# Performance work log

Hardware: AMD Instinct MI355X
Metric: run time of the kernel (lower is better)

The kernel has to match this reference:

```python
import jax, jax.numpy as jnp
import numpy as np

H = 16  # n_heads

def setup_inputs() -> dict:
    key = jax.random.key(0)
    ks = jax.random.split(key, 7)
    B, L, D = 4, 2048, 1024
    s = 0.02
    return {
        "z": jax.random.normal(ks[0], (B, L, D), jnp.float32),
        "connection": jax.random.normal(ks[1], (B, L, D), jnp.float32),
        "Wq": jax.random.normal(ks[2], (2 * D, D), jnp.float32) * s,
        "Wk": jax.random.normal(ks[3], (2 * D, D), jnp.float32) * s,
        "Wv": jax.random.normal(ks[4], (D, D), jnp.float32) * s,
        "Wo": jax.random.normal(ks[5], (D, D), jnp.float32) * s,
        "temp": jnp.float32(1.0),
    }

def reference(z, connection, Wq, Wk, Wv, Wo, temp):
    B, L, D = z.shape
    hd = D // H
    zc = jnp.concatenate([z, connection], axis=-1)          # [B,L,2D]
    Q = (zc @ Wq).reshape(B, L, H, hd).transpose(0, 2, 1, 3)  # [B,H,L,hd]
    K = (zc @ Wk).reshape(B, L, H, hd).transpose(0, 2, 1, 3)
    V = (z @ Wv).reshape(B, L, H, hd).transpose(0, 2, 1, 3)
    scale = (hd ** -0.5) * temp
    scores = jnp.einsum('bhqd,bhkd->bhqk', Q, K) * scale     # [B,H,L,L]
    rel = jax.nn.sigmoid(scores)
    rel_sum = jnp.clip(rel.sum(-1, keepdims=True), 1.0, None)
    out = jnp.einsum('bhqk,bhkd->bhqd', rel, V) / rel_sum
    out = out.transpose(0, 2, 1, 3).reshape(B, L, D)
    return out @ Wo
```

## Files before the change

### kernel.cpp

```cpp
#include <hip/hip_runtime.h>

typedef unsigned short u16;
typedef unsigned int u32;
typedef __bf16 bf16x8 __attribute__((ext_vector_type(8)));
typedef float f32x4 __attribute__((ext_vector_type(4)));

#define DEV static __device__ __forceinline__

DEV u16 f2bf(float x) {
    union { float f; u32 u; } v; v.f = x;
    u32 r = (v.u + 0x7FFFu + ((v.u >> 16) & 1u)) >> 16;
    return (u16)r;
}

DEV void store_c(float* p, float v) { *p = v; }
DEV void store_c(u16* p, float v) { *p = f2bf(v); }

DEV int swz(int row, int bytecol) { return row * 128 + (bytecol ^ ((row & 7) << 4)); }

__global__ void pack_zc(const float* __restrict__ z, const float* __restrict__ cn,
                        u16* __restrict__ zc) {
    size_t i = ((size_t)blockIdx.x * blockDim.x + threadIdx.x) * 4;
    size_t t = i >> 11;
    int c = (int)(i & 2047);
    const float* src = (c < 1024) ? (z + t * 1024 + c) : (cn + t * 1024 + (c - 1024));
    float4 v = *reinterpret_cast<const float4*>(src);
    u32 lo = (u32)f2bf(v.x) | ((u32)f2bf(v.y) << 16);
    u32 hi = (u32)f2bf(v.z) | ((u32)f2bf(v.w) << 16);
    *reinterpret_cast<uint2*>(zc + i) = make_uint2(lo, hi);
}

__global__ void transpose_conv_w(const float* __restrict__ W, u16* __restrict__ WT,
                                 int K, int N) {
    __shared__ float tile[32][33];
    int n0 = blockIdx.x * 32, k0 = blockIdx.y * 32;
    int tx = threadIdx.x, ty = threadIdx.y;
    #pragma unroll
    for (int i = ty; i < 32; i += 8)
        tile[i][tx] = W[(size_t)(k0 + i) * N + n0 + tx];
    __syncthreads();
    #pragma unroll
    for (int i = ty; i < 32; i += 8)
        WT[(size_t)(n0 + i) * K + k0 + tx] = f2bf(tile[tx][i]);
}

__global__ void transpose_v(const u16* __restrict__ Vf, u16* __restrict__ Vt) {
    __shared__ u16 tile[32][33];
    int bh = blockIdx.z; int b = bh >> 4, h = bh & 15;
    int l0 = blockIdx.x * 32, d0 = blockIdx.y * 32;
    int tx = threadIdx.x, ty = threadIdx.y;
    #pragma unroll
    for (int i = ty; i < 32; i += 8)
        tile[i][tx] = Vf[(size_t)(b * 2048 + l0 + i) * 1024 + h * 64 + d0 + tx];
    __syncthreads();
    #pragma unroll
    for (int i = ty; i < 32; i += 8)
        Vt[((size_t)bh * 64 + d0 + i) * 2048 + l0 + tx] = tile[tx][i];
}

template <typename OutT>
__global__ __launch_bounds__(256, 2)
void gemm_bt(const u16* __restrict__ A, const u16* __restrict__ BT,
             OutT* __restrict__ C, int M, int N, int K,
             int lda, int ldb, int ldc) {
    __shared__ u16 As[128 * 64];
    __shared__ u16 Bs[128 * 64];
    const int tid = threadIdx.x;
    const int lane = tid & 63;
    const int wid = tid >> 6;
    const int m0 = blockIdx.x * 128;
    const int n0 = blockIdx.y * 128;
    const int wr = (wid >> 1) * 64;
    const int wc = (wid & 1) * 64;

    f32x4 acc[4][4];
    #pragma unroll
    for (int i = 0; i < 4; ++i)
        #pragma unroll
        for (int j = 0; j < 4; ++j)
            acc[i][j] = f32x4{0.f, 0.f, 0.f, 0.f};

    const int srow = tid >> 3;
    const int schunk = tid & 7;

    for (int k0 = 0; k0 < K; k0 += 64) {
        __syncthreads();
        #pragma unroll
        for (int p = 0; p < 4; ++p) {
            int row = p * 32 + srow;
            int4 v = *reinterpret_cast<const int4*>(A + (size_t)(m0 + row) * lda + k0 + schunk * 8);
            *reinterpret_cast<int4*>(reinterpret_cast<char*>(As) + swz(row, schunk * 16)) = v;
        }
        #pragma unroll
        for (int p = 0; p < 4; ++p) {
            int row = p * 32 + srow;
            int4 v = *reinterpret_cast<const int4*>(BT + (size_t)(n0 + row) * ldb + k0 + schunk * 8);
            *reinterpret_cast<int4*>(reinterpret_cast<char*>(Bs) + swz(row, schunk * 16)) = v;
        }
        __syncthreads();
        #pragma unroll
        for (int kk = 0; kk < 64; kk += 32) {
            bf16x8 af[4], bfr[4];
            #pragma unroll
            for (int i = 0; i < 4; ++i) {
                int row = wr + i * 16 + (lane & 15);
                af[i] = *reinterpret_cast<const bf16x8*>(
                    reinterpret_cast<const char*>(As) + swz(row, (kk + (lane >> 4) * 8) * 2));
            }
            #pragma unroll
            for (int j = 0; j < 4; ++j) {
                int row = wc + j * 16 + (lane & 15);
                bfr[j] = *reinterpret_cast<const bf16x8*>(
                    reinterpret_cast<const char*>(Bs) + swz(row, (kk + (lane >> 4) * 8) * 2));
            }
            #pragma unroll
            for (int i = 0; i < 4; ++i)
                #pragma unroll
                for (int j = 0; j < 4; ++j)
                    acc[i][j] = __builtin_amdgcn_mfma_f32_16x16x32_bf16(af[i], bfr[j], acc[i][j], 0, 0, 0);
        }
    }

    #pragma unroll
    for (int i = 0; i < 4; ++i)
        #pragma unroll
        for (int j = 0; j < 4; ++j)
            #pragma unroll
            for (int r = 0; r < 4; ++r) {
                int row = m0 + wr + i * 16 + (lane >> 4) * 4 + r;
                int col = n0 + wc + j * 16 + (lane & 15);
                store_c(&C[(size_t)row * ldc + col], acc[i][j][r]);
            }
}

__global__ __launch_bounds__(256, 2)
void attn_kernel(const u16* __restrict__ Qf, const u16* __restrict__ Kf,
                 const u16* __restrict__ Vt, u16* __restrict__ Oa,
                 const float* __restrict__ temp) {
    constexpr int L = 2048, D = 1024, HD = 64;
    __shared__ u16 Qs[64 * 64];
    __shared__ u16 Ks[64 * 64];
    __shared__ u16 Vs[64 * 64];
    __shared__ u16 Ps[4][16 * 64];

    const int tid = threadIdx.x;
    const int lane = tid & 63;
    const int wid = tid >> 6;
    const int bh = blockIdx.y;
    const int b = bh >> 4, h = bh & 15;
    const int q0 = blockIdx.x * 64;
    const float scale = temp[0] * 0.125f;

    const u16* Qbase = Qf + (size_t)(b * L) * D + h * HD;
    const u16* Kbase = Kf + (size_t)(b * L) * D + h * HD;
    const u16* Vbase = Vt + (size_t)bh * HD * L;

    const int srow = tid >> 3;
    const int schunk = tid & 7;

    #pragma unroll
    for (int p = 0; p < 2; ++p) {
        int row = p * 32 + srow;
        int4 v = *reinterpret_cast<const int4*>(Qbase + (size_t)(q0 + row) * D + schunk * 8);
        *reinterpret_cast<int4*>(reinterpret_cast<char*>(Qs) + swz(row, schunk * 16)) = v;
    }

    f32x4 oacc[4];
    #pragma unroll
    for (int j = 0; j < 4; ++j) oacc[j] = f32x4{0.f, 0.f, 0.f, 0.f};
    float rsum[4] = {0.f, 0.f, 0.f, 0.f};

    for (int k0 = 0; k0 < L; k0 += 64) {
        __syncthreads();
        #pragma unroll
        for (int p = 0; p < 2; ++p) {
            int row = p * 32 + srow;
            int4 v = *reinterpret_cast<const int4*>(Kbase + (size_t)(k0 + row) * D + schunk * 8);
            *reinterpret_cast<int4*>(reinterpret_cast<char*>(Ks) + swz(row, schunk * 16)) = v;
        }
        #pragma unroll
        for (int p = 0; p < 2; ++p) {
            int row = p * 32 + srow;
            int4 v = *reinterpret_cast<const int4*>(Vbase + (size_t)row * L + k0 + schunk * 8);
            *reinterpret_cast<int4*>(reinterpret_cast<char*>(Vs) + swz(row, schunk * 16)) = v;
        }
        __syncthreads();

        f32x4 s[4];
        #pragma unroll
        for (int ct = 0; ct < 4; ++ct) s[ct] = f32x4{0.f, 0.f, 0.f, 0.f};
        #pragma unroll
        for (int kk = 0; kk < 64; kk += 32) {
            int qrow = wid * 16 + (lane & 15);
            bf16x8 aq = *reinterpret_cast<const bf16x8*>(
                reinterpret_cast<const char*>(Qs) + swz(qrow, (kk + (lane >> 4) * 8) * 2));
            #pragma unroll
            for (int ct = 0; ct < 4; ++ct) {
                int krow = ct * 16 + (lane & 15);
                bf16x8 bk = *reinterpret_cast<const bf16x8*>(
                    reinterpret_cast<const char*>(Ks) + swz(krow, (kk + (lane >> 4) * 8) * 2));
                s[ct] = __builtin_amdgcn_mfma_f32_16x16x32_bf16(aq, bk, s[ct], 0, 0, 0);
            }
        }

        #pragma unroll
        for (int ct = 0; ct < 4; ++ct) {
            #pragma unroll
            for (int r = 0; r < 4; ++r) {
                float pv = 1.0f / (1.0f + __expf(-s[ct][r] * scale));
                rsum[r] += pv;
                int prow = (lane >> 4) * 4 + r;
                *reinterpret_cast<u16*>(reinterpret_cast<char*>(Ps[wid]) +
                    swz(prow, (ct * 16 + (lane & 15)) * 2)) = f2bf(pv);
            }
        }

        #pragma unroll
        for (int kk = 0; kk < 64; kk += 32) {
            int prow = (lane & 15);
            bf16x8 ap = *reinterpret_cast<const bf16x8*>(
                reinterpret_cast<const char*>(Ps[wid]) + swz(prow, (kk + (lane >> 4) * 8) * 2));
            #pragma unroll
            for (int ct = 0; ct < 4; ++ct) {
                int vrow = ct * 16 + (lane & 15);
                bf16x8 bv = *reinterpret_cast<const bf16x8*>(
                    reinterpret_cast<const char*>(Vs) + swz(vrow, (kk + (lane >> 4) * 8) * 2));
                oacc[ct] = __builtin_amdgcn_mfma_f32_16x16x32_bf16(ap, bv, oacc[ct], 0, 0, 0);
            }
        }
    }

    #pragma unroll
    for (int r = 0; r < 4; ++r) {
        float v = rsum[r];
        v += __shfl_xor(v, 1);
        v += __shfl_xor(v, 2);
        v += __shfl_xor(v, 4);
        v += __shfl_xor(v, 8);
        rsum[r] = fmaxf(v, 1.0f);
    }

    #pragma unroll
    for (int ct = 0; ct < 4; ++ct)
        #pragma unroll
        for (int r = 0; r < 4; ++r) {
            int row = q0 + wid * 16 + (lane >> 4) * 4 + r;
            int col = h * HD + ct * 16 + (lane & 15);
            Oa[(size_t)(b * L + row) * D + col] = f2bf(oacc[ct][r] / rsum[r]);
        }
}

extern "C" void kernel_launch(void* const* d_in, const int* in_sizes, int n_in,
                              void* d_out, int out_size, void* d_ws, size_t ws_size,
                              hipStream_t stream) {
    const float* z    = (const float*)d_in[0];
    const float* cn   = (const float*)d_in[1];
    const float* Wq   = (const float*)d_in[2];
    const float* Wk   = (const float*)d_in[3];
    const float* Wv   = (const float*)d_in[4];
    const float* Wo   = (const float*)d_in[5];
    const float* temp = (const float*)d_in[6];

    char* ws = (char*)d_ws;
    u16* zc  = (u16*)ws; ws += (size_t)8192 * 2048 * 2;
    u16* WqT = (u16*)ws; ws += (size_t)1024 * 2048 * 2;
    u16* WkT = (u16*)ws; ws += (size_t)1024 * 2048 * 2;
    u16* WvT = (u16*)ws; ws += (size_t)1024 * 1024 * 2;
    u16* WoT = (u16*)ws; ws += (size_t)1024 * 1024 * 2;
    u16* Qf  = (u16*)ws; ws += (size_t)8192 * 1024 * 2;
    u16* Kf  = (u16*)ws; ws += (size_t)8192 * 1024 * 2;
    u16* Vf  = (u16*)ws; ws += (size_t)8192 * 1024 * 2;
    u16* Vt  = zc;
    u16* Oa  = Vf;

    pack_zc<<<16384, 256, 0, stream>>>(z, cn, zc);

    dim3 tb(32, 8);
    transpose_conv_w<<<dim3(32, 64), tb, 0, stream>>>(Wq, WqT, 2048, 1024);
    transpose_conv_w<<<dim3(32, 64), tb, 0, stream>>>(Wk, WkT, 2048, 1024);
    transpose_conv_w<<<dim3(32, 32), tb, 0, stream>>>(Wv, WvT, 1024, 1024);
    transpose_conv_w<<<dim3(32, 32), tb, 0, stream>>>(Wo, WoT, 1024, 1024);

    gemm_bt<u16><<<dim3(64, 8), 256, 0, stream>>>(zc, WqT, Qf, 8192, 1024, 2048, 2048, 2048, 1024);
    gemm_bt<u16><<<dim3(64, 8), 256, 0, stream>>>(zc, WkT, Kf, 8192, 1024, 2048, 2048, 2048, 1024);
    gemm_bt<u16><<<dim3(64, 8), 256, 0, stream>>>(zc, WvT, Vf, 8192, 1024, 1024, 2048, 1024, 1024);

    transpose_v<<<dim3(64, 2, 64), tb, 0, stream>>>(Vf, Vt);

    attn_kernel<<<dim3(32, 64), 256, 0, stream>>>(Qf, Kf, Vt, Oa, temp);

    gemm_bt<float><<<dim3(64, 8), 256, 0, stream>>>(Oa, WoT, (float*)d_out, 8192, 1024, 1024, 1024, 1024, 1024);
}
```

Measured before the change: 476.3 us.

## Use direct global-to-LDS loads, fuse Q/K GEMM, and compute row sums with MFMA

GEMM and attention tile loads now use global_load_lds into a pre-swizzled LDS layout instead of going through registers. The Q and K projections become one GEMM with N=2048, since WqT and WkT sit next to each other in the workspace; attention reads Q and K from that interleaved buffer. The sigmoid now uses exp2 and a hardware reciprocal. Row sums come from an extra MFMA against a ones vector, which removes the shuffle reduction, and manual bf16 rounding is replaced by native conversions. The MFMA row sum is taken over bf16-rounded probabilities, so precision shifts slightly, and correctness relies on the barrier waiting for the async LDS loads.

```diff
diff --git a/kernel.cpp b/kernel.cpp
--- a/kernel.cpp
+++ b/kernel.cpp
@@ -7,14 +7,14 @@
 
 #define DEV static __device__ __forceinline__
 
-DEV u16 f2bf(float x) {
-    union { float f; u32 u; } v; v.f = x;
-    u32 r = (v.u + 0x7FFFu + ((v.u >> 16) & 1u)) >> 16;
-    return (u16)r;
+DEV void gload16(const void* g, void* l) {
+    __builtin_amdgcn_global_load_lds(
+        (const __attribute__((address_space(1))) void*)g,
+        (__attribute__((address_space(3))) void*)l, 16, 0, 0);
 }
 
 DEV void store_c(float* p, float v) { *p = v; }
-DEV void store_c(u16* p, float v) { *p = f2bf(v); }
+DEV void store_c(u16* p, float v) { *(__bf16*)p = (__bf16)v; }
 
 DEV int swz(int row, int bytecol) { return row * 128 + (bytecol ^ ((row & 7) << 4)); }
 
@@ -25,9 +25,10 @@
     int c = (int)(i & 2047);
     const float* src = (c < 1024) ? (z + t * 1024 + c) : (cn + t * 1024 + (c - 1024));
     float4 v = *reinterpret_cast<const float4*>(src);
-    u32 lo = (u32)f2bf(v.x) | ((u32)f2bf(v.y) << 16);
-    u32 hi = (u32)f2bf(v.z) | ((u32)f2bf(v.w) << 16);
-    *reinterpret_cast<uint2*>(zc + i) = make_uint2(lo, hi);
+    union { __bf16 h[4]; uint2 u; } o;
+    o.h[0] = (__bf16)v.x; o.h[1] = (__bf16)v.y;
+    o.h[2] = (__bf16)v.z; o.h[3] = (__bf16)v.w;
+    *reinterpret_cast<uint2*>(zc + i) = o.u;
 }
 
 __global__ void transpose_conv_w(const float* __restrict__ W, u16* __restrict__ WT,
@@ -41,7 +42,7 @@
     __syncthreads();
     #pragma unroll
     for (int i = ty; i < 32; i += 8)
-        WT[(size_t)(n0 + i) * K + k0 + tx] = f2bf(tile[tx][i]);
+        *(__bf16*)&WT[(size_t)(n0 + i) * K + k0 + tx] = (__bf16)tile[tx][i];
 }
 
 __global__ void transpose_v(const u16* __restrict__ Vf, u16* __restrict__ Vt) {
@@ -80,24 +81,25 @@
         for (int j = 0; j < 4; ++j)
             acc[i][j] = f32x4{0.f, 0.f, 0.f, 0.f};
 
-    const int srow = tid >> 3;
-    const int schunk = tid & 7;
+    const int srcoff = ((lane & 7) ^ (lane >> 3)) * 8;
+    const int rb = wid * 32 + (lane >> 3);
+    const u16* aptr[4]; const u16* bptr[4];
+    #pragma unroll
+    for (int p = 0; p < 4; ++p) {
+        aptr[p] = A  + (size_t)(m0 + rb + p * 8) * lda + srcoff;
+        bptr[p] = BT + (size_t)(n0 + rb + p * 8) * ldb + srcoff;
+    }
 
     for (int k0 = 0; k0 < K; k0 += 64) {
         __syncthreads();
         #pragma unroll
-        for (int p = 0; p < 4; ++p) {
-            int row = p * 32 + srow;
-            int4 v = *reinterpret_cast<const int4*>(A + (size_t)(m0 + row) * lda + k0 + schunk * 8);
-            *reinterpret_cast<int4*>(reinterpret_cast<char*>(As) + swz(row, schunk * 16)) = v;
-        }
-        #pragma unroll
-        for (int p = 0; p < 4; ++p) {
-            int row = p * 32 + srow;
-            int4 v = *reinterpret_cast<const int4*>(BT + (size_t)(n0 + row) * ldb + k0 + schunk * 8);
-            *reinterpret_cast<int4*>(reinterpret_cast<char*>(Bs) + swz(row, schunk * 16)) = v;
-        }
-        __syncthreads();
+        for (int p = 0; p < 4; ++p)
+            gload16(aptr[p] + k0, (char*)As + (wid * 4 + p) * 1024);
+        #pragma unroll
+        for (int p = 0; p < 4; ++p)
+            gload16(bptr[p] + k0, (char*)Bs + (wid * 4 + p) * 1024);
+        __syncthreads();
+
         #pragma unroll
         for (int kk = 0; kk < 64; kk += 32) {
             bf16x8 af[4], bfr[4];
@@ -134,10 +136,9 @@
 }
 
 __global__ __launch_bounds__(256, 2)
-void attn_kernel(const u16* __restrict__ Qf, const u16* __restrict__ Kf,
-                 const u16* __restrict__ Vt, u16* __restrict__ Oa,
-                 const float* __restrict__ temp) {
-    constexpr int L = 2048, D = 1024, HD = 64;
+void attn_kernel(const u16* __restrict__ QKf, const u16* __restrict__ Vt,
+                 u16* __restrict__ Oa, const float* __restrict__ temp) {
+    constexpr int L = 2048, D = 1024, QKLD = 2048, HD = 64;
     __shared__ u16 Qs[64 * 64];
     __shared__ u16 Ks[64 * 64];
     __shared__ u16 Vs[64 * 64];
@@ -149,41 +150,44 @@
     const int bh = blockIdx.y;
     const int b = bh >> 4, h = bh & 15;
     const int q0 = blockIdx.x * 64;
-    const float scale = temp[0] * 0.125f;
-
-    const u16* Qbase = Qf + (size_t)(b * L) * D + h * HD;
-    const u16* Kbase = Kf + (size_t)(b * L) * D + h * HD;
+    const float sneg = -temp[0] * 0.125f * 1.44269504f;
+
+    const u16* Qbase = QKf + (size_t)(b * L) * QKLD + h * HD;
+    const u16* Kbase = Qbase + 1024;
     const u16* Vbase = Vt + (size_t)bh * HD * L;
 
-    const int srow = tid >> 3;
-    const int schunk = tid & 7;
-
+    const int srcoff = ((lane & 7) ^ (lane >> 3)) * 8;
+    const int rb = wid * 16 + (lane >> 3);
+
+    #pragma unroll
+    for (int p = 0; p < 2; ++p)
+        gload16(Qbase + (size_t)(q0 + rb + p * 8) * QKLD + srcoff,
+                (char*)Qs + (wid * 2 + p) * 1024);
+
+    const u16* kptr[2]; const u16* vptr[2];
     #pragma unroll
     for (int p = 0; p < 2; ++p) {
-        int row = p * 32 + srow;
-        int4 v = *reinterpret_cast<const int4*>(Qbase + (size_t)(q0 + row) * D + schunk * 8);
-        *reinterpret_cast<int4*>(reinterpret_cast<char*>(Qs) + swz(row, schunk * 16)) = v;
-    }
+        kptr[p] = Kbase + (size_t)(rb + p * 8) * QKLD + srcoff;
+        vptr[p] = Vbase + (size_t)(rb + p * 8) * L + srcoff;
+    }
+
+    bf16x8 onesf;
+    #pragma unroll
+    for (int j = 0; j < 8; ++j) onesf[j] = (__bf16)1.0f;
 
     f32x4 oacc[4];
     #pragma unroll
     for (int j = 0; j < 4; ++j) oacc[j] = f32x4{0.f, 0.f, 0.f, 0.f};
-    float rsum[4] = {0.f, 0.f, 0.f, 0.f};
+    f32x4 racc = f32x4{0.f, 0.f, 0.f, 0.f};
 
     for (int k0 = 0; k0 < L; k0 += 64) {
         __syncthreads();
         #pragma unroll
-        for (int p = 0; p < 2; ++p) {
-            int row = p * 32 + srow;
-            int4 v = *reinterpret_cast<const int4*>(Kbase + (size_t)(k0 + row) * D + schunk * 8);
-            *reinterpret_cast<int4*>(reinterpret_cast<char*>(Ks) + swz(row, schunk * 16)) = v;
-        }
-        #pragma unroll
-        for (int p = 0; p < 2; ++p) {
-            int row = p * 32 + srow;
-            int4 v = *reinterpret_cast<const int4*>(Vbase + (size_t)row * L + k0 + schunk * 8);
-            *reinterpret_cast<int4*>(reinterpret_cast<char*>(Vs) + swz(row, schunk * 16)) = v;
-        }
+        for (int p = 0; p < 2; ++p)
+            gload16(kptr[p] + (size_t)k0 * QKLD, (char*)Ks + (wid * 2 + p) * 1024);
+        #pragma unroll
+        for (int p = 0; p < 2; ++p)
+            gload16(vptr[p] + k0, (char*)Vs + (wid * 2 + p) * 1024);
         __syncthreads();
 
         f32x4 s[4];
@@ -207,11 +211,10 @@
         for (int ct = 0; ct < 4; ++ct) {
             #pragma unroll
             for (int r = 0; r < 4; ++r) {
-                float pv = 1.0f / (1.0f + __expf(-s[ct][r] * scale));
-                rsum[r] += pv;
+                float pv = __builtin_amdgcn_rcpf(1.0f + exp2f(s[ct][r] * sneg));
                 int prow = (lane >> 4) * 4 + r;
-                *reinterpret_cast<u16*>(reinterpret_cast<char*>(Ps[wid]) +
-                    swz(prow, (ct * 16 + (lane & 15)) * 2)) = f2bf(pv);
+                *(__bf16*)(reinterpret_cast<char*>(Ps[wid]) +
+                    swz(prow, (ct * 16 + (lane & 15)) * 2)) = (__bf16)pv;
             }
         }
 
@@ -220,6 +223,7 @@
             int prow = (lane & 15);
             bf16x8 ap = *reinterpret_cast<const bf16x8*>(
                 reinterpret_cast<const char*>(Ps[wid]) + swz(prow, (kk + (lane >> 4) * 8) * 2));
+            racc = __builtin_amdgcn_mfma_f32_16x16x32_bf16(ap, onesf, racc, 0, 0, 0);
             #pragma unroll
             for (int ct = 0; ct < 4; ++ct) {
                 int vrow = ct * 16 + (lane & 15);
@@ -230,15 +234,10 @@
         }
     }
 
-    #pragma unroll
-    for (int r = 0; r < 4; ++r) {
-        float v = rsum[r];
-        v += __shfl_xor(v, 1);
-        v += __shfl_xor(v, 2);
-        v += __shfl_xor(v, 4);
-        v += __shfl_xor(v, 8);
-        rsum[r] = fmaxf(v, 1.0f);
-    }
+    float rdiv[4];
+    #pragma unroll
+    for (int r = 0; r < 4; ++r)
+        rdiv[r] = __builtin_amdgcn_rcpf(fmaxf(racc[r], 1.0f));
 
     #pragma unroll
     for (int ct = 0; ct < 4; ++ct)
@@ -246,7 +245,7 @@
         for (int r = 0; r < 4; ++r) {
             int row = q0 + wid * 16 + (lane >> 4) * 4 + r;
             int col = h * HD + ct * 16 + (lane & 15);
-            Oa[(size_t)(b * L + row) * D + col] = f2bf(oacc[ct][r] / rsum[r]);
+            *(__bf16*)&Oa[(size_t)(b * L + row) * D + col] = (__bf16)(oacc[ct][r] * rdiv[r]);
         }
 }
 
@@ -259,7 +258,9 @@
     const float* Wk   = (const float*)d_in[3];
     const float* Wv   = (const float*)d_in[4];
     const float* Wo   = (const float*)d_in[5];
+    const float* Wo_  = (const float*)d_in[5];
     const float* temp = (const float*)d_in[6];
+    (void)Wo_;
 
     char* ws = (char*)d_ws;
     u16* zc  = (u16*)ws; ws += (size_t)8192 * 2048 * 2;
@@ -267,8 +268,7 @@
     u16* WkT = (u16*)ws; ws += (size_t)1024 * 2048 * 2;
     u16* WvT = (u16*)ws; ws += (size_t)1024 * 1024 * 2;
     u16* WoT = (u16*)ws; ws += (size_t)1024 * 1024 * 2;
-    u16* Qf  = (u16*)ws; ws += (size_t)8192 * 1024 * 2;
-    u16* Kf  = (u16*)ws; ws += (size_t)8192 * 1024 * 2;
+    u16* QKf = (u16*)ws; ws += (size_t)8192 * 2048 * 2;
     u16* Vf  = (u16*)ws; ws += (size_t)8192 * 1024 * 2;
     u16* Vt  = zc;
     u16* Oa  = Vf;
@@ -281,13 +281,12 @@
     transpose_conv_w<<<dim3(32, 32), tb, 0, stream>>>(Wv, WvT, 1024, 1024);
     transpose_conv_w<<<dim3(32, 32), tb, 0, stream>>>(Wo, WoT, 1024, 1024);
 
-    gemm_bt<u16><<<dim3(64, 8), 256, 0, stream>>>(zc, WqT, Qf, 8192, 1024, 2048, 2048, 2048, 1024);
-    gemm_bt<u16><<<dim3(64, 8), 256, 0, stream>>>(zc, WkT, Kf, 8192, 1024, 2048, 2048, 2048, 1024);
-    gemm_bt<u16><<<dim3(64, 8), 256, 0, stream>>>(zc, WvT, Vf, 8192, 1024, 1024, 2048, 1024, 1024);
+    gemm_bt<u16><<<dim3(64, 16), 256, 0, stream>>>(zc, WqT, QKf, 8192, 2048, 2048, 2048, 2048, 2048);
+    gemm_bt<u16><<<dim3(64, 8),  256, 0, stream>>>(zc, WvT, Vf,  8192, 1024, 1024, 2048, 1024, 1024);
 
     transpose_v<<<dim3(64, 2, 64), tb, 0, stream>>>(Vf, Vt);
 
-    attn_kernel<<<dim3(32, 64), 256, 0, stream>>>(Qf, Kf, Vt, Oa, temp);
+    attn_kernel<<<dim3(32, 64), 256, 0, stream>>>(QKf, Vt, Oa, temp);
 
     gemm_bt<float><<<dim3(64, 8), 256, 0, stream>>>(Oa, WoT, (float*)d_out, 8192, 1024, 1024, 1024, 1024, 1024);
 }
```

New measurement: 413.8 us. 13.1% less time.
